# Kernel optimization log

Hardware: AMD Instinct MI355X
Metric: run time of the kernel (lower is better)

The kernel has to match this reference:

```python
import jax, jax.numpy as jnp
import numpy as np

N = 50000
E = 400000
IN_CH = 256
HEADS = 4
OUT_CH = 64
HID = HEADS * OUT_CH  # 256
ALPHA = 0.2
LN_EPS = 1e-5


def setup_inputs() -> dict:
    key = jax.random.key(0)
    ks = jax.random.split(key, 8)
    h = jax.random.normal(ks[0], (N, IN_CH), dtype=jnp.float32)
    edge_row = jax.random.randint(ks[1], (E,), 0, N, dtype=jnp.int32)
    edge_col = jax.random.randint(ks[2], (E,), 0, N, dtype=jnp.int32)
    # xavier-uniform-ish params
    def xavier(k, shape, fan_in, fan_out):
        lim = np.sqrt(6.0 / (fan_in + fan_out)).astype(np.float32)
        return jax.random.uniform(k, shape, jnp.float32, -lim, lim)
    W = xavier(ks[3], (IN_CH, HID), IN_CH, HID)              # Linear no bias
    attn_fc = xavier(ks[4], (HEADS, 2 * OUT_CH), 2 * OUT_CH, 1)
    ln_gamma = jnp.ones((HID,), jnp.float32)
    ln_beta = jnp.zeros((HID,), jnp.float32)
    ffn_w = xavier(ks[5], (HID, HID), HID, HID)
    ffn_b = jnp.zeros((HID,), jnp.float32)
    return {"h": h, "edge_row": edge_row, "edge_col": edge_col,
            "W": W, "attn_fc": attn_fc, "ln_gamma": ln_gamma,
            "ln_beta": ln_beta, "ffn_w": ffn_w, "ffn_b": ffn_b}


def reference(h, edge_row, edge_col, W, attn_fc, ln_gamma, ln_beta, ffn_w, ffn_b):
    # Wh: [N, H, D]
    Wh = (h @ W).reshape(N, HEADS, OUT_CH)
    Wh_i = Wh[edge_row]   # [E, H, D]
    Wh_j = Wh[edge_col]   # [E, H, D]
    # e = leakyrelu(cat(Wh_i, Wh_j) . attn_fc) per head -> split contraction
    a_src = attn_fc[:, :OUT_CH]  # [H, D]
    a_dst = attn_fc[:, OUT_CH:]  # [H, D]
    e = jnp.einsum('ehd,hd->eh', Wh_i, a_src) + jnp.einsum('ehd,hd->eh', Wh_j, a_dst)
    e = jax.nn.leaky_relu(e, negative_slope=ALPHA)
    # global max-shift exp (matches torch.exp(e - e.max(dim=0)))
    e = jnp.exp(e - jnp.max(e, axis=0, keepdims=True))  # [E, H]
    e_sum = jax.ops.segment_sum(e, edge_row, num_segments=N)  # [N, H]
    alpha = e / (e_sum[edge_row] + 1e-15)  # [E, H]  (dropout = identity in eval)
    # scatter-add weighted messages
    h_new = jax.ops.segment_sum(Wh_j * alpha[..., None], edge_row, num_segments=N)
    h_new = h_new.reshape(N, HID) + Wh.reshape(N, HID)  # residual (shapes match)
    # LayerNorm
    mu = jnp.mean(h_new, axis=-1, keepdims=True)
    var = jnp.var(h_new, axis=-1, keepdims=True)
    h_new = (h_new - mu) * jax.lax.rsqrt(var + LN_EPS) * ln_gamma + ln_beta
    # FFN: Linear + ReLU (+ dropout identity)
    return jax.nn.relu(h_new @ ffn_w + ffn_b)
```

## Files before the change

### kernel.cpp

```cpp
#include <hip/hip_runtime.h>
#include <hip/hip_bf16.h>

#define N_NODES 50000
#define E_EDGES 400000
#define IN_CH   256
#define HEADS   4
#define OUT_CH  64
#define HID     256
#define ALPHA   0.2f
#define LN_EPS  1e-5f

using f32x4  = __attribute__((ext_vector_type(4))) float;
using bf16x8 = __attribute__((ext_vector_type(8))) short;
using u16x8  = __attribute__((ext_vector_type(8))) unsigned short;
using u16x4  = __attribute__((ext_vector_type(4))) unsigned short;

__device__ __forceinline__ unsigned short f2bf(float f) {
    __hip_bfloat16 b = __float2bfloat16(f);
    return *(unsigned short*)&b;
}
__device__ __forceinline__ float bf2f(unsigned short u) {
    __hip_bfloat16 b = *(__hip_bfloat16*)&u;
    return __bfloat162float(b);
}

__global__ __launch_bounds__(256) void prep_kernel(
    const float* __restrict__ W, const float* __restrict__ ffn_w,
    unsigned short* __restrict__ Wt, unsigned short* __restrict__ Ft)
{
    int i = blockIdx.x * 256 + threadIdx.x;
    if (i < 65536) {
        int n = i >> 8, k = i & 255;
        Wt[i] = f2bf(W[k * 256 + n]);
    } else {
        int j = i - 65536;
        int n = j >> 8, k = j & 255;
        Ft[j] = f2bf(ffn_w[k * 256 + n]);
    }
}

template<bool A_IS_F32, bool RELU_BIAS>
__global__ __launch_bounds__(256) void gemm_mfma(
    const void* __restrict__ Av, const unsigned short* __restrict__ Bt,
    const float* __restrict__ bias, void* __restrict__ Cv, int M)
{
    constexpr int K = 256, BM = 128, BK = 64;
    __shared__ unsigned short As[BM * BK];
    __shared__ unsigned short Bs[BM * BK];

    const int bx = blockIdx.x & 1;
    const int by = blockIdx.x >> 1;
    const int row0 = by * BM, col0 = bx * 128;
    const int tid = threadIdx.x;
    const int lane = tid & 63, wid = tid >> 6;
    const int wr = wid >> 1, wc = wid & 1;
    const int lm = lane & 15, lk = lane >> 4;

    f32x4 acc[4][4] = {};

    for (int k0 = 0; k0 < K; k0 += BK) {
        if (A_IS_F32) {
            const float* A = (const float*)Av;
            #pragma unroll
            for (int i = 0; i < 8; i++) {
                int lin = tid + i * 256;
                int r = lin >> 4, c4 = lin & 15;
                int gr = row0 + r;
                float4 v = make_float4(0.f, 0.f, 0.f, 0.f);
                if (gr < M) v = *(const float4*)(A + (size_t)gr * K + k0 + c4 * 4);
                uint2 p;
                p.x = (unsigned)f2bf(v.x) | ((unsigned)f2bf(v.y) << 16);
                p.y = (unsigned)f2bf(v.z) | ((unsigned)f2bf(v.w) << 16);
                *(uint2*)((char*)As + r * 128 + ((c4 * 8) ^ ((r & 7) << 4))) = p;
            }
        } else {
            const unsigned short* A = (const unsigned short*)Av;
            #pragma unroll
            for (int i = 0; i < 4; i++) {
                int lin = tid + i * 256;
                int r = lin >> 3, c8 = lin & 7;
                int gr = row0 + r;
                u16x8 v = {};
                if (gr < M) v = *(const u16x8*)(A + (size_t)gr * K + k0 + c8 * 8);
                *(u16x8*)((char*)As + r * 128 + ((c8 * 16) ^ ((r & 7) << 4))) = v;
            }
        }
        #pragma unroll
        for (int i = 0; i < 4; i++) {
            int lin = tid + i * 256;
            int r = lin >> 3, c8 = lin & 7;
            u16x8 v = *(const u16x8*)(Bt + (size_t)(col0 + r) * K + k0 + c8 * 8);
            *(u16x8*)((char*)Bs + r * 128 + ((c8 * 16) ^ ((r & 7) << 4))) = v;
        }
        __syncthreads();

        #pragma unroll
        for (int kk = 0; kk < 2; kk++) {
            bf16x8 a[4], b[4];
            #pragma unroll
            for (int i = 0; i < 4; i++) {
                int m = wr * 64 + i * 16 + lm;
                a[i] = *(const bf16x8*)((const char*)As + m * 128 +
                        ((kk * 64 + lk * 16) ^ ((m & 7) << 4)));
            }
            #pragma unroll
            for (int j = 0; j < 4; j++) {
                int n = wc * 64 + j * 16 + lm;
                b[j] = *(const bf16x8*)((const char*)Bs + n * 128 +
                        ((kk * 64 + lk * 16) ^ ((n & 7) << 4)));
            }
            #pragma unroll
            for (int i = 0; i < 4; i++)
                #pragma unroll
                for (int j = 0; j < 4; j++)
                    acc[i][j] = __builtin_amdgcn_mfma_f32_16x16x32_bf16(
                        a[i], b[j], acc[i][j], 0, 0, 0);
        }
        __syncthreads();
    }

    #pragma unroll
    for (int j = 0; j < 4; j++) {
        int gc = col0 + wc * 64 + j * 16 + lm;
        float bv = RELU_BIAS ? bias[gc] : 0.f;
        #pragma unroll
        for (int i = 0; i < 4; i++) {
            int gr0 = row0 + wr * 64 + i * 16 + lk * 4;
            #pragma unroll
            for (int q = 0; q < 4; q++) {
                int gr = gr0 + q;
                if (gr >= M) continue;
                float v = acc[i][j][q];
                if (RELU_BIAS) {
                    v += bv; v = v > 0.f ? v : 0.f;
                    ((float*)Cv)[(size_t)gr * 256 + gc] = v;
                } else {
                    ((unsigned short*)Cv)[(size_t)gr * 256 + gc] = f2bf(v);
                }
            }
        }
    }
}

__global__ __launch_bounds__(256) void scores_kernel(
    const unsigned short* __restrict__ Wh, const float* __restrict__ attn_fc,
    float* __restrict__ s_src, float* __restrict__ s_dst)
{
    const int lane = threadIdx.x & 63, wid = threadIdx.x >> 6;
    const int n = blockIdx.x * 4 + wid;
    const int h = lane >> 4;
    const int d0 = 4 * (lane & 15);
    u16x4 w = *(const u16x4*)(Wh + (size_t)n * HID + 4 * lane);
    float ps = 0.f, pd = 0.f;
    #pragma unroll
    for (int q = 0; q < 4; q++) {
        float wf = bf2f(w[q]);
        ps += wf * attn_fc[h * 128 + d0 + q];
        pd += wf * attn_fc[h * 128 + 64 + d0 + q];
    }
    #pragma unroll
    for (int off = 8; off; off >>= 1) {
        ps += __shfl_xor(ps, off, 16);
        pd += __shfl_xor(pd, off, 16);
    }
    if ((lane & 15) == 0) {
        s_src[n * HEADS + h] = ps;
        s_dst[n * HEADS + h] = pd;
    }
}

__global__ void hist_kernel(const int* __restrict__ erow, int* __restrict__ counts) {
    int e = blockIdx.x * blockDim.x + threadIdx.x;
    if (e < E_EDGES) atomicAdd(&counts[erow[e]], 1);
}

__global__ __launch_bounds__(256) void scanA_kernel(
    const int* __restrict__ counts, int* __restrict__ bsum)
{
    const int b = blockIdx.x, tid = threadIdx.x;
    int i0 = b * 512 + tid;
    int v = 0;
    if (i0 < N_NODES) v += counts[i0];
    if (i0 + 256 < N_NODES) v += counts[i0 + 256];
    #pragma unroll
    for (int off = 32; off; off >>= 1) v += __shfl_xor(v, off, 64);
    __shared__ int ws[4];
    if ((tid & 63) == 0) ws[tid >> 6] = v;
    __syncthreads();
    if (tid == 0) bsum[b] = ws[0] + ws[1] + ws[2] + ws[3];
}

__global__ __launch_bounds__(128) void scanB_kernel(
    const int* __restrict__ bsum, int* __restrict__ bscan, int nb)
{
    const int tid = threadIdx.x;
    const int lane = tid & 63, wid = tid >> 6;
    int val = (tid < nb) ? bsum[tid] : 0;
    int x = val;
    #pragma unroll
    for (int off = 1; off < 64; off <<= 1) {
        int y = __shfl_up(x, off, 64);
        if (lane >= off) x += y;
    }
    __shared__ int w0;
    if (tid == 63) w0 = x;
    __syncthreads();
    if (wid == 1) x += w0;
    if (tid < nb) bscan[tid] = x - val;
}

__global__ __launch_bounds__(512) void scanC_kernel(
    const int* __restrict__ counts, const int* __restrict__ bscan,
    int* __restrict__ offsets, int* __restrict__ cursor)
{
    const int b = blockIdx.x, tid = threadIdx.x;
    const int lane = tid & 63, wid = tid >> 6;
    const int i = b * 512 + tid;
    int v = (i < N_NODES) ? counts[i] : 0;
    int x = v;
    #pragma unroll
    for (int off = 1; off < 64; off <<= 1) {
        int y = __shfl_up(x, off, 64);
        if (lane >= off) x += y;
    }
    __shared__ int ws[8];
    if (lane == 63) ws[wid] = x;
    __syncthreads();
    if (wid == 0 && lane < 8) {
        int s = ws[lane];
        #pragma unroll
        for (int off = 1; off < 8; off <<= 1) {
            int y = __shfl_up(s, off, 8);
            if ((lane & 7) >= off) s += y;
        }
        ws[lane] = s;
    }
    __syncthreads();
    int prefix = (wid ? ws[wid - 1] : 0) + bscan[b];
    int excl = prefix + x - v;
    if (i < N_NODES) { offsets[i] = excl; cursor[i] = excl; }
    if (i == N_NODES - 1) offsets[N_NODES] = excl + v;
}

__global__ __launch_bounds__(256) void scatter_kernel(
    const int* __restrict__ erow, const int* __restrict__ ecol,
    const float* __restrict__ s_src, const float* __restrict__ s_dst,
    int* __restrict__ cursor, int* __restrict__ sorted_col,
    float4* __restrict__ sorted_w)
{
    int e = blockIdx.x * blockDim.x + threadIdx.x;
    if (e >= E_EDGES) return;
    int r = erow[e], c = ecol[e];
    float4 ss = ((const float4*)s_src)[r];
    float4 sd = ((const float4*)s_dst)[c];
    float sc[4] = {ss.x + sd.x, ss.y + sd.y, ss.z + sd.z, ss.w + sd.w};
    float4 w;
    float* wp = (float*)&w;
    #pragma unroll
    for (int h = 0; h < 4; h++) {
        float v = sc[h] > 0.f ? sc[h] : ALPHA * sc[h];
        wp[h] = __expf(v);
    }
    int pos = atomicAdd(&cursor[r], 1);
    sorted_col[pos] = c;
    sorted_w[pos] = w;
}

__global__ __launch_bounds__(256) void aggregate_ln_kernel(
    const unsigned short* __restrict__ Wh, const float* __restrict__ sorted_w,
    const int* __restrict__ offsets, const int* __restrict__ sorted_col,
    const float* __restrict__ ln_gamma, const float* __restrict__ ln_beta,
    unsigned short* __restrict__ h_ln)
{
    const int lane = threadIdx.x & 63, wid = threadIdx.x >> 6;
    const int n = blockIdx.x * 4 + wid;
    const int h = lane >> 4;
    const int c0 = 4 * lane;
    const int beg = offsets[n], end = offsets[n + 1];

    float acc[4] = {0.f, 0.f, 0.f, 0.f};
    float wsum = 0.f;
    for (int base = beg; base < end; base += 64) {
        int cnt = min(64, end - base);
        int cv = (base + lane < end) ? sorted_col[base + lane] : 0;
        #pragma unroll 2
        for (int jj = 0; jj < cnt; jj++) {
            float w = sorted_w[(base + jj) * 4 + h];
            int c = __shfl(cv, jj, 64);
            u16x4 wr = *(const u16x4*)(Wh + (size_t)c * HID + c0);
            wsum += w;
            #pragma unroll
            for (int q = 0; q < 4; q++) acc[q] += w * bf2f(wr[q]);
        }
    }
    u16x4 rr = *(const u16x4*)(Wh + (size_t)n * HID + c0);
    float inv_w = 1.f / (wsum + 1e-15f);
    float val[4];
    #pragma unroll
    for (int q = 0; q < 4; q++) val[q] = acc[q] * inv_w + bf2f(rr[q]);

    float s = val[0] + val[1] + val[2] + val[3];
    #pragma unroll
    for (int off = 32; off; off >>= 1) s += __shfl_xor(s, off, 64);
    float mu = s * (1.f / HID);
    float s2 = 0.f;
    #pragma unroll
    for (int q = 0; q < 4; q++) { float d = val[q] - mu; s2 += d * d; }
    #pragma unroll
    for (int off = 32; off; off >>= 1) s2 += __shfl_xor(s2, off, 64);
    float inv_std = rsqrtf(s2 * (1.f / HID) + LN_EPS);

    float4 g = *(const float4*)(ln_gamma + c0);
    float4 bb = *(const float4*)(ln_beta + c0);
    u16x4 outv;
    outv[0] = f2bf((val[0] - mu) * inv_std * g.x + bb.x);
    outv[1] = f2bf((val[1] - mu) * inv_std * g.y + bb.y);
    outv[2] = f2bf((val[2] - mu) * inv_std * g.z + bb.z);
    outv[3] = f2bf((val[3] - mu) * inv_std * g.w + bb.w);
    *(u16x4*)(h_ln + (size_t)n * HID + c0) = outv;
}

extern "C" void kernel_launch(void* const* d_in, const int* in_sizes, int n_in,
                              void* d_out, int out_size, void* d_ws, size_t ws_size,
                              hipStream_t stream)
{
    const float* h        = (const float*)d_in[0];
    const int*   erow     = (const int*)  d_in[1];
    const int*   ecol     = (const int*)  d_in[2];
    const float* W        = (const float*)d_in[3];
    const float* attn_fc  = (const float*)d_in[4];
    const float* ln_gamma = (const float*)d_in[5];
    const float* ln_beta  = (const float*)d_in[6];
    const float* ffn_w    = (const float*)d_in[7];
    const float* ffn_b    = (const float*)d_in[8];
    float* out = (float*)d_out;

    unsigned short* Wh   = (unsigned short*)d_ws;
    unsigned short* h_ln = Wh + (size_t)N_NODES * HID;
    unsigned short* Wt   = h_ln + (size_t)N_NODES * HID;
    unsigned short* Ft   = Wt + 65536;
    float* s_src  = (float*)(Ft + 65536);
    float* s_dst  = s_src + N_NODES * HEADS;
    float* sorted_w = s_dst + N_NODES * HEADS;
    int*   counts = (int*)(sorted_w + (size_t)E_EDGES * HEADS);
    int*   offsets = counts + N_NODES;
    int*   cursor  = offsets + N_NODES + 1;
    int*   sorted_col = cursor + N_NODES;
    int*   bsum   = sorted_col + E_EDGES;
    int*   bscan  = bsum + 128;

    const int NB = (N_NODES + 511) / 512;

    hipMemsetAsync(counts, 0, N_NODES * sizeof(int), stream);
    prep_kernel<<<512, 256, 0, stream>>>(W, ffn_w, Wt, Ft);

    gemm_mfma<true, false><<<((N_NODES + 127) / 128) * 2, 256, 0, stream>>>(
        h, Wt, nullptr, Wh, N_NODES);

    scores_kernel<<<N_NODES / 4, 256, 0, stream>>>(Wh, attn_fc, s_src, s_dst);
    hist_kernel<<<(E_EDGES + 255) / 256, 256, 0, stream>>>(erow, counts);
    scanA_kernel<<<NB, 256, 0, stream>>>(counts, bsum);
    scanB_kernel<<<1, 128, 0, stream>>>(bsum, bscan, NB);
    scanC_kernel<<<NB, 512, 0, stream>>>(counts, bscan, offsets, cursor);
    scatter_kernel<<<(E_EDGES + 255) / 256, 256, 0, stream>>>(
        erow, ecol, s_src, s_dst, cursor, sorted_col, (float4*)sorted_w);
    aggregate_ln_kernel<<<N_NODES / 4, 256, 0, stream>>>(
        Wh, sorted_w, offsets, sorted_col, ln_gamma, ln_beta, h_ln);

    gemm_mfma<false, true><<<((N_NODES + 127) / 128) * 2, 256, 0, stream>>>(
        h_ln, Ft, ffn_b, out, N_NODES);
}
```

Before: 281.6 us.

## Fuse attention score computation into GEMM epilogue and double-buffer LDS with direct loads

```diff
diff --git a/kernel.cpp b/kernel.cpp
--- a/kernel.cpp
+++ b/kernel.cpp
@@ -15,6 +15,9 @@
 using u16x8  = __attribute__((ext_vector_type(8))) unsigned short;
 using u16x4  = __attribute__((ext_vector_type(4))) unsigned short;
 
+typedef __attribute__((address_space(3))) void* lds_vp;
+typedef const __attribute__((address_space(1))) void* gbl_vp;
+
 __device__ __forceinline__ unsigned short f2bf(float f) {
     __hip_bfloat16 b = __float2bfloat16(f);
     return *(unsigned short*)&b;
@@ -39,18 +42,20 @@
     }
 }
 
-template<bool A_IS_F32, bool RELU_BIAS>
+template<bool A_IS_F32, bool RELU_BIAS, bool SCORES>
 __global__ __launch_bounds__(256) void gemm_mfma(
     const void* __restrict__ Av, const unsigned short* __restrict__ Bt,
-    const float* __restrict__ bias, void* __restrict__ Cv, int M)
-{
-    constexpr int K = 256, BM = 128, BK = 64;
-    __shared__ unsigned short As[BM * BK];
-    __shared__ unsigned short Bs[BM * BK];
+    const float* __restrict__ bias, const float* __restrict__ attn_fc,
+    void* __restrict__ Cv, float* __restrict__ s_src, float* __restrict__ s_dst,
+    int M)
+{
+    constexpr int K = 256, BK = 64, NT = K / BK;
+    __shared__ unsigned short As[2][128 * 64];
+    __shared__ unsigned short Bs[2][128 * 64];
 
     const int bx = blockIdx.x & 1;
     const int by = blockIdx.x >> 1;
-    const int row0 = by * BM, col0 = bx * 128;
+    const int row0 = by * 128, col0 = bx * 128;
     const int tid = threadIdx.x;
     const int lane = tid & 63, wid = tid >> 6;
     const int wr = wid >> 1, wc = wid & 1;
@@ -58,55 +63,62 @@
 
     f32x4 acc[4][4] = {};
 
-    for (int k0 = 0; k0 < K; k0 += BK) {
-        if (A_IS_F32) {
-            const float* A = (const float*)Av;
-            #pragma unroll
-            for (int i = 0; i < 8; i++) {
-                int lin = tid + i * 256;
-                int r = lin >> 4, c4 = lin & 15;
-                int gr = row0 + r;
-                float4 v = make_float4(0.f, 0.f, 0.f, 0.f);
-                if (gr < M) v = *(const float4*)(A + (size_t)gr * K + k0 + c4 * 4);
-                uint2 p;
-                p.x = (unsigned)f2bf(v.x) | ((unsigned)f2bf(v.y) << 16);
-                p.y = (unsigned)f2bf(v.z) | ((unsigned)f2bf(v.w) << 16);
-                *(uint2*)((char*)As + r * 128 + ((c4 * 8) ^ ((r & 7) << 4))) = p;
-            }
-        } else {
-            const unsigned short* A = (const unsigned short*)Av;
-            #pragma unroll
-            for (int i = 0; i < 4; i++) {
-                int lin = tid + i * 256;
-                int r = lin >> 3, c8 = lin & 7;
-                int gr = row0 + r;
-                u16x8 v = {};
-                if (gr < M) v = *(const u16x8*)(A + (size_t)gr * K + k0 + c8 * 8);
-                *(u16x8*)((char*)As + r * 128 + ((c8 * 16) ^ ((r & 7) << 4))) = v;
-            }
-        }
+    auto stageB = [&](int buf, int k0) {
         #pragma unroll
         for (int i = 0; i < 4; i++) {
+            int lin = wid * 64 + lane + i * 256;
+            int r = lin >> 3, c8 = lin & 7;
+            int c8s = c8 ^ (r & 7);
+            const unsigned short* g = Bt + (size_t)(col0 + r) * K + k0 + c8s * 8;
+            __builtin_amdgcn_global_load_lds((gbl_vp)g,
+                (lds_vp)&Bs[buf][(size_t)(i * 256 + wid * 64) * 8], 16, 0, 0);
+        }
+    };
+    auto stageA_bf16 = [&](int buf, int k0) {
+        const unsigned short* A = (const unsigned short*)Av;
+        #pragma unroll
+        for (int i = 0; i < 4; i++) {
+            int lin = wid * 64 + lane + i * 256;
+            int r = lin >> 3, c8 = lin & 7;
+            int c8s = c8 ^ (r & 7);
+            const unsigned short* g = A + (size_t)(row0 + r) * K + k0 + c8s * 8;
+            __builtin_amdgcn_global_load_lds((gbl_vp)g,
+                (lds_vp)&As[buf][(size_t)(i * 256 + wid * 64) * 8], 16, 0, 0);
+        }
+    };
+    auto stageA_f32 = [&](int buf, int k0) {
+        const float* A = (const float*)Av;
+        #pragma unroll
+        for (int i = 0; i < 8; i++) {
             int lin = tid + i * 256;
-            int r = lin >> 3, c8 = lin & 7;
-            u16x8 v = *(const u16x8*)(Bt + (size_t)(col0 + r) * K + k0 + c8 * 8);
-            *(u16x8*)((char*)Bs + r * 128 + ((c8 * 16) ^ ((r & 7) << 4))) = v;
-        }
-        __syncthreads();
-
+            int r = lin >> 4, c4 = lin & 15;
+            int gr = row0 + r;
+            float4 v = make_float4(0.f, 0.f, 0.f, 0.f);
+            if (gr < M) v = *(const float4*)(A + (size_t)gr * K + k0 + c4 * 4);
+            uint2 p;
+            p.x = (unsigned)f2bf(v.x) | ((unsigned)f2bf(v.y) << 16);
+            p.y = (unsigned)f2bf(v.z) | ((unsigned)f2bf(v.w) << 16);
+            *(uint2*)((char*)&As[buf][0] + r * 128 + ((c4 * 8) ^ ((r & 7) << 4))) = p;
+        }
+    };
+    auto stage = [&](int buf, int k0) {
+        if (A_IS_F32) stageA_f32(buf, k0); else stageA_bf16(buf, k0);
+        stageB(buf, k0);
+    };
+    auto compute = [&](int buf) {
         #pragma unroll
         for (int kk = 0; kk < 2; kk++) {
             bf16x8 a[4], b[4];
             #pragma unroll
             for (int i = 0; i < 4; i++) {
                 int m = wr * 64 + i * 16 + lm;
-                a[i] = *(const bf16x8*)((const char*)As + m * 128 +
+                a[i] = *(const bf16x8*)((const char*)&As[buf][0] + m * 128 +
                         ((kk * 64 + lk * 16) ^ ((m & 7) << 4)));
             }
             #pragma unroll
             for (int j = 0; j < 4; j++) {
                 int n = wc * 64 + j * 16 + lm;
-                b[j] = *(const bf16x8*)((const char*)Bs + n * 128 +
+                b[j] = *(const bf16x8*)((const char*)&Bs[buf][0] + n * 128 +
                         ((kk * 64 + lk * 16) ^ ((n & 7) << 4)));
             }
             #pragma unroll
@@ -116,6 +128,14 @@
                     acc[i][j] = __builtin_amdgcn_mfma_f32_16x16x32_bf16(
                         a[i], b[j], acc[i][j], 0, 0, 0);
         }
+    };
+
+    stage(0, 0);
+    __syncthreads();
+    #pragma unroll
+    for (int t = 0; t < NT; t++) {
+        if (t + 1 < NT) stage((t + 1) & 1, (t + 1) * BK);
+        compute(t & 1);
         __syncthreads();
     }
 
@@ -140,32 +160,37 @@
             }
         }
     }
-}
-
-__global__ __launch_bounds__(256) void scores_kernel(
-    const unsigned short* __restrict__ Wh, const float* __restrict__ attn_fc,
-    float* __restrict__ s_src, float* __restrict__ s_dst)
-{
-    const int lane = threadIdx.x & 63, wid = threadIdx.x >> 6;
-    const int n = blockIdx.x * 4 + wid;
-    const int h = lane >> 4;
-    const int d0 = 4 * (lane & 15);
-    u16x4 w = *(const u16x4*)(Wh + (size_t)n * HID + 4 * lane);
-    float ps = 0.f, pd = 0.f;
-    #pragma unroll
-    for (int q = 0; q < 4; q++) {
-        float wf = bf2f(w[q]);
-        ps += wf * attn_fc[h * 128 + d0 + q];
-        pd += wf * attn_fc[h * 128 + 64 + d0 + q];
-    }
-    #pragma unroll
-    for (int off = 8; off; off >>= 1) {
-        ps += __shfl_xor(ps, off, 16);
-        pd += __shfl_xor(pd, off, 16);
-    }
-    if ((lane & 15) == 0) {
-        s_src[n * HEADS + h] = ps;
-        s_dst[n * HEADS + h] = pd;
+
+    if (SCORES) {
+        const int head = bx * 2 + wc;
+        float as[4], ad[4];
+        #pragma unroll
+        for (int j = 0; j < 4; j++) {
+            as[j] = attn_fc[head * 128 + j * 16 + lm];
+            ad[j] = attn_fc[head * 128 + 64 + j * 16 + lm];
+        }
+        #pragma unroll
+        for (int i = 0; i < 4; i++) {
+            #pragma unroll
+            for (int q = 0; q < 4; q++) {
+                float ps = 0.f, pd = 0.f;
+                #pragma unroll
+                for (int j = 0; j < 4; j++) {
+                    ps += acc[i][j][q] * as[j];
+                    pd += acc[i][j][q] * ad[j];
+                }
+                #pragma unroll
+                for (int off = 8; off; off >>= 1) {
+                    ps += __shfl_xor(ps, off, 16);
+                    pd += __shfl_xor(pd, off, 16);
+                }
+                int gr = row0 + wr * 64 + i * 16 + lk * 4 + q;
+                if (lm == 0 && gr < M) {
+                    s_src[gr * HEADS + head] = ps;
+                    s_dst[gr * HEADS + head] = pd;
+                }
+            }
+        }
     }
 }
 
@@ -354,10 +379,9 @@
     hipMemsetAsync(counts, 0, N_NODES * sizeof(int), stream);
     prep_kernel<<<512, 256, 0, stream>>>(W, ffn_w, Wt, Ft);
 
-    gemm_mfma<true, false><<<((N_NODES + 127) / 128) * 2, 256, 0, stream>>>(
-        h, Wt, nullptr, Wh, N_NODES);
-
-    scores_kernel<<<N_NODES / 4, 256, 0, stream>>>(Wh, attn_fc, s_src, s_dst);
+    gemm_mfma<true, false, true><<<((N_NODES + 127) / 128) * 2, 256, 0, stream>>>(
+        h, Wt, nullptr, attn_fc, Wh, s_src, s_dst, N_NODES);
+
     hist_kernel<<<(E_EDGES + 255) / 256, 256, 0, stream>>>(erow, counts);
     scanA_kernel<<<NB, 256, 0, stream>>>(counts, bsum);
     scanB_kernel<<<1, 128, 0, stream>>>(bsum, bscan, NB);
@@ -367,6 +391,6 @@
     aggregate_ln_kernel<<<N_NODES / 4, 256, 0, stream>>>(
         Wh, sorted_w, offsets, sorted_col, ln_gamma, ln_beta, h_ln);
 
-    gemm_mfma<false, true><<<((N_NODES + 127) / 128) * 2, 256, 0, stream>>>(
-        h_ln, Ft, ffn_b, out, N_NODES);
-}
+    gemm_mfma<false, true, false><<<((N_NODES + 127) / 128) * 2, 256, 0, stream>>>(
+        h_ln, Ft, ffn_b, nullptr, out, nullptr, nullptr, N_NODES);
+}
```

New measurement: 276.5 us. No clear change (-1.8%).

## Use persistent B-resident MFMA GEMM and process two edges per wave in aggregation

Applied to the files above, without the earlier changes.

```diff
diff --git a/kernel.cpp b/kernel.cpp
--- a/kernel.cpp
+++ b/kernel.cpp
@@ -10,10 +10,13 @@
 #define ALPHA   0.2f
 #define LN_EPS  1e-5f
 
-using f32x4  = __attribute__((ext_vector_type(4))) float;
+using f32x16 = __attribute__((ext_vector_type(16))) float;
 using bf16x8 = __attribute__((ext_vector_type(8))) short;
 using u16x8  = __attribute__((ext_vector_type(8))) unsigned short;
 using u16x4  = __attribute__((ext_vector_type(4))) unsigned short;
+
+typedef __attribute__((address_space(3))) void* lds_vp;
+typedef const __attribute__((address_space(1))) void* gbl_vp;
 
 __device__ __forceinline__ unsigned short f2bf(float f) {
     __hip_bfloat16 b = __float2bfloat16(f);
@@ -40,103 +43,92 @@
 }
 
 template<bool A_IS_F32, bool RELU_BIAS>
-__global__ __launch_bounds__(256) void gemm_mfma(
+__global__ __launch_bounds__(512, 2) void gemm_bres(
     const void* __restrict__ Av, const unsigned short* __restrict__ Bt,
     const float* __restrict__ bias, void* __restrict__ Cv, int M)
 {
-    constexpr int K = 256, BM = 128, BK = 64;
-    __shared__ unsigned short As[BM * BK];
-    __shared__ unsigned short Bs[BM * BK];
-
-    const int bx = blockIdx.x & 1;
-    const int by = blockIdx.x >> 1;
-    const int row0 = by * BM, col0 = bx * 128;
+    __shared__ unsigned short Bs[256 * 256];
+
     const int tid = threadIdx.x;
     const int lane = tid & 63, wid = tid >> 6;
-    const int wr = wid >> 1, wc = wid & 1;
-    const int lm = lane & 15, lk = lane >> 4;
-
-    f32x4 acc[4][4] = {};
-
-    for (int k0 = 0; k0 < K; k0 += BK) {
+
+    #pragma unroll
+    for (int i = 0; i < 16; i++) {
+        int d = i * 512 + tid;
+        int n = d >> 5, cp = d & 31;
+        int cs = cp ^ (n & 31);
+        const unsigned short* g = Bt + (size_t)n * 256 + cs * 8;
+        __builtin_amdgcn_global_load_lds((gbl_vp)g, (lds_vp)&Bs[(size_t)d * 8],
+                                         16, 0, 0);
+    }
+    __syncthreads();
+
+    const int strip = wid * 256 + blockIdx.x;
+    const int r0 = strip * 32;
+    if (r0 >= M) return;
+
+    const int q5 = lane & 31, kg = lane >> 5;
+    const int rowc = min(r0 + q5, M - 1);
+
+    f32x16 acc[8] = {};
+
+    const float* Af = (const float*)Av;
+    const unsigned short* Ab = (const unsigned short*)Av;
+
+    float4 ra0, ra1; u16x8 rab;
+    if (A_IS_F32) {
+        const float* p = Af + (size_t)rowc * 256 + kg * 8;
+        ra0 = *(const float4*)p; ra1 = *(const float4*)(p + 4);
+    } else {
+        rab = *(const u16x8*)(Ab + (size_t)rowc * 256 + kg * 8);
+    }
+
+    #pragma unroll 2
+    for (int t = 0; t < 16; t++) {
+        float4 nb0, nb1; u16x8 nbb;
+        if (t + 1 < 16) {
+            if (A_IS_F32) {
+                const float* p = Af + (size_t)rowc * 256 + (t + 1) * 16 + kg * 8;
+                nb0 = *(const float4*)p; nb1 = *(const float4*)(p + 4);
+            } else {
+                nbb = *(const u16x8*)(Ab + (size_t)rowc * 256 + (t + 1) * 16 + kg * 8);
+            }
+        }
+        bf16x8 af;
         if (A_IS_F32) {
-            const float* A = (const float*)Av;
-            #pragma unroll
-            for (int i = 0; i < 8; i++) {
-                int lin = tid + i * 256;
-                int r = lin >> 4, c4 = lin & 15;
-                int gr = row0 + r;
-                float4 v = make_float4(0.f, 0.f, 0.f, 0.f);
-                if (gr < M) v = *(const float4*)(A + (size_t)gr * K + k0 + c4 * 4);
-                uint2 p;
-                p.x = (unsigned)f2bf(v.x) | ((unsigned)f2bf(v.y) << 16);
-                p.y = (unsigned)f2bf(v.z) | ((unsigned)f2bf(v.w) << 16);
-                *(uint2*)((char*)As + r * 128 + ((c4 * 8) ^ ((r & 7) << 4))) = p;
-            }
+            union { unsigned int u[4]; bf16x8 v; } cv;
+            cv.u[0] = (unsigned)f2bf(ra0.x) | ((unsigned)f2bf(ra0.y) << 16);
+            cv.u[1] = (unsigned)f2bf(ra0.z) | ((unsigned)f2bf(ra0.w) << 16);
+            cv.u[2] = (unsigned)f2bf(ra1.x) | ((unsigned)f2bf(ra1.y) << 16);
+            cv.u[3] = (unsigned)f2bf(ra1.z) | ((unsigned)f2bf(ra1.w) << 16);
+            af = cv.v;
         } else {
-            const unsigned short* A = (const unsigned short*)Av;
-            #pragma unroll
-            for (int i = 0; i < 4; i++) {
-                int lin = tid + i * 256;
-                int r = lin >> 3, c8 = lin & 7;
-                int gr = row0 + r;
-                u16x8 v = {};
-                if (gr < M) v = *(const u16x8*)(A + (size_t)gr * K + k0 + c8 * 8);
-                *(u16x8*)((char*)As + r * 128 + ((c8 * 16) ^ ((r & 7) << 4))) = v;
-            }
+            union { u16x8 u; bf16x8 v; } cv; cv.u = rab; af = cv.v;
         }
         #pragma unroll
-        for (int i = 0; i < 4; i++) {
-            int lin = tid + i * 256;
-            int r = lin >> 3, c8 = lin & 7;
-            u16x8 v = *(const u16x8*)(Bt + (size_t)(col0 + r) * K + k0 + c8 * 8);
-            *(u16x8*)((char*)Bs + r * 128 + ((c8 * 16) ^ ((r & 7) << 4))) = v;
-        }
-        __syncthreads();
-
-        #pragma unroll
-        for (int kk = 0; kk < 2; kk++) {
-            bf16x8 a[4], b[4];
-            #pragma unroll
-            for (int i = 0; i < 4; i++) {
-                int m = wr * 64 + i * 16 + lm;
-                a[i] = *(const bf16x8*)((const char*)As + m * 128 +
-                        ((kk * 64 + lk * 16) ^ ((m & 7) << 4)));
-            }
-            #pragma unroll
-            for (int j = 0; j < 4; j++) {
-                int n = wc * 64 + j * 16 + lm;
-                b[j] = *(const bf16x8*)((const char*)Bs + n * 128 +
-                        ((kk * 64 + lk * 16) ^ ((n & 7) << 4)));
-            }
-            #pragma unroll
-            for (int i = 0; i < 4; i++)
-                #pragma unroll
-                for (int j = 0; j < 4; j++)
-                    acc[i][j] = __builtin_amdgcn_mfma_f32_16x16x32_bf16(
-                        a[i], b[j], acc[i][j], 0, 0, 0);
-        }
-        __syncthreads();
-    }
-
-    #pragma unroll
-    for (int j = 0; j < 4; j++) {
-        int gc = col0 + wc * 64 + j * 16 + lm;
+        for (int n = 0; n < 8; n++) {
+            const bf16x8 bf = *(const bf16x8*)((const char*)Bs +
+                (size_t)(n * 32 + q5) * 512 + (((t * 2 + kg) ^ q5) * 16));
+            acc[n] = __builtin_amdgcn_mfma_f32_32x32x16_bf16(af, bf, acc[n], 0, 0, 0);
+        }
+        ra0 = nb0; ra1 = nb1; rab = nbb;
+    }
+
+    #pragma unroll
+    for (int n = 0; n < 8; n++) {
+        int gc = n * 32 + q5;
         float bv = RELU_BIAS ? bias[gc] : 0.f;
         #pragma unroll
-        for (int i = 0; i < 4; i++) {
-            int gr0 = row0 + wr * 64 + i * 16 + lk * 4;
-            #pragma unroll
-            for (int q = 0; q < 4; q++) {
-                int gr = gr0 + q;
-                if (gr >= M) continue;
-                float v = acc[i][j][q];
-                if (RELU_BIAS) {
-                    v += bv; v = v > 0.f ? v : 0.f;
-                    ((float*)Cv)[(size_t)gr * 256 + gc] = v;
-                } else {
-                    ((unsigned short*)Cv)[(size_t)gr * 256 + gc] = f2bf(v);
-                }
+        for (int reg = 0; reg < 16; reg++) {
+            int rl = (reg & 3) + 8 * (reg >> 2) + 4 * kg;
+            int gr = r0 + rl;
+            if (gr >= M) continue;
+            float v = acc[n][reg];
+            if (RELU_BIAS) {
+                v += bv; v = v > 0.f ? v : 0.f;
+                ((float*)Cv)[(size_t)gr * 256 + gc] = v;
+            } else {
+                ((unsigned short*)Cv)[(size_t)gr * 256 + gc] = f2bf(v);
             }
         }
     }
@@ -274,50 +266,77 @@
 {
     const int lane = threadIdx.x & 63, wid = threadIdx.x >> 6;
     const int n = blockIdx.x * 4 + wid;
-    const int h = lane >> 4;
-    const int c0 = 4 * lane;
+    const int p = lane >> 5;
+    const int q5 = lane & 31;
+    const int c0 = q5 * 8;
+    const int h = q5 >> 3;
     const int beg = offsets[n], end = offsets[n + 1];
 
-    float acc[4] = {0.f, 0.f, 0.f, 0.f};
+    float acc[8] = {};
     float wsum = 0.f;
     for (int base = beg; base < end; base += 64) {
         int cnt = min(64, end - base);
         int cv = (base + lane < end) ? sorted_col[base + lane] : 0;
+        int jj = 0;
         #pragma unroll 2
-        for (int jj = 0; jj < cnt; jj++) {
-            float w = sorted_w[(base + jj) * 4 + h];
-            int c = __shfl(cv, jj, 64);
-            u16x4 wr = *(const u16x4*)(Wh + (size_t)c * HID + c0);
+        for (; jj + 2 <= cnt; jj += 2) {
+            int c = __shfl(cv, jj + p, 64);
+            float w = sorted_w[(size_t)(base + jj + p) * 4 + h];
+            u16x8 r = *(const u16x8*)(Wh + (size_t)c * HID + c0);
             wsum += w;
             #pragma unroll
-            for (int q = 0; q < 4; q++) acc[q] += w * bf2f(wr[q]);
-        }
-    }
-    u16x4 rr = *(const u16x4*)(Wh + (size_t)n * HID + c0);
+            for (int k = 0; k < 8; k++) acc[k] += w * bf2f(r[k]);
+        }
+        if (jj < cnt) {
+            int c = __shfl(cv, jj, 64);
+            if (p == 0) {
+                float w = sorted_w[(size_t)(base + jj) * 4 + h];
+                u16x8 r = *(const u16x8*)(Wh + (size_t)c * HID + c0);
+                wsum += w;
+                #pragma unroll
+                for (int k = 0; k < 8; k++) acc[k] += w * bf2f(r[k]);
+            }
+        }
+    }
+    wsum += __shfl_xor(wsum, 32, 64);
+    #pragma unroll
+    for (int k = 0; k < 8; k++) acc[k] += __shfl_xor(acc[k], 32, 64);
+
+    u16x8 rr = *(const u16x8*)(Wh + (size_t)n * HID + c0);
     float inv_w = 1.f / (wsum + 1e-15f);
-    float val[4];
-    #pragma unroll
-    for (int q = 0; q < 4; q++) val[q] = acc[q] * inv_w + bf2f(rr[q]);
-
-    float s = val[0] + val[1] + val[2] + val[3];
-    #pragma unroll
-    for (int off = 32; off; off >>= 1) s += __shfl_xor(s, off, 64);
+    float val[8];
+    float s = 0.f;
+    #pragma unroll
+    for (int k = 0; k < 8; k++) {
+        val[k] = acc[k] * inv_w + bf2f(rr[k]);
+        s += val[k];
+    }
+    #pragma unroll
+    for (int off = 16; off; off >>= 1) s += __shfl_xor(s, off, 64);
     float mu = s * (1.f / HID);
     float s2 = 0.f;
     #pragma unroll
-    for (int q = 0; q < 4; q++) { float d = val[q] - mu; s2 += d * d; }
-    #pragma unroll
-    for (int off = 32; off; off >>= 1) s2 += __shfl_xor(s2, off, 64);
+    for (int k = 0; k < 8; k++) { float d = val[k] - mu; s2 += d * d; }
+    #pragma unroll
+    for (int off = 16; off; off >>= 1) s2 += __shfl_xor(s2, off, 64);
     float inv_std = rsqrtf(s2 * (1.f / HID) + LN_EPS);
 
-    float4 g = *(const float4*)(ln_gamma + c0);
-    float4 bb = *(const float4*)(ln_beta + c0);
-    u16x4 outv;
-    outv[0] = f2bf((val[0] - mu) * inv_std * g.x + bb.x);
-    outv[1] = f2bf((val[1] - mu) * inv_std * g.y + bb.y);
-    outv[2] = f2bf((val[2] - mu) * inv_std * g.z + bb.z);
-    outv[3] = f2bf((val[3] - mu) * inv_std * g.w + bb.w);
-    *(u16x4*)(h_ln + (size_t)n * HID + c0) = outv;
+    if (p == 0) {
+        float4 g0 = *(const float4*)(ln_gamma + c0);
+        float4 g1 = *(const float4*)(ln_gamma + c0 + 4);
+        float4 b0 = *(const float4*)(ln_beta + c0);
+        float4 b1 = *(const float4*)(ln_beta + c0 + 4);
+        u16x8 outv;
+        outv[0] = f2bf((val[0] - mu) * inv_std * g0.x + b0.x);
+        outv[1] = f2bf((val[1] - mu) * inv_std * g0.y + b0.y);
+        outv[2] = f2bf((val[2] - mu) * inv_std * g0.z + b0.z);
+        outv[3] = f2bf((val[3] - mu) * inv_std * g0.w + b0.w);
+        outv[4] = f2bf((val[4] - mu) * inv_std * g1.x + b1.x);
+        outv[5] = f2bf((val[5] - mu) * inv_std * g1.y + b1.y);
+        outv[6] = f2bf((val[6] - mu) * inv_std * g1.z + b1.z);
+        outv[7] = f2bf((val[7] - mu) * inv_std * g1.w + b1.w);
+        *(u16x8*)(h_ln + (size_t)n * HID + c0) = outv;
+    }
 }
 
 extern "C" void kernel_launch(void* const* d_in, const int* in_sizes, int n_in,
@@ -354,8 +373,7 @@
     hipMemsetAsync(counts, 0, N_NODES * sizeof(int), stream);
     prep_kernel<<<512, 256, 0, stream>>>(W, ffn_w, Wt, Ft);
 
-    gemm_mfma<true, false><<<((N_NODES + 127) / 128) * 2, 256, 0, stream>>>(
-        h, Wt, nullptr, Wh, N_NODES);
+    gemm_bres<true, false><<<256, 512, 0, stream>>>(h, Wt, nullptr, Wh, N_NODES);
 
     scores_kernel<<<N_NODES / 4, 256, 0, stream>>>(Wh, attn_fc, s_src, s_dst);
     hist_kernel<<<(E_EDGES + 255) / 256, 256, 0, stream>>>(erow, counts);
@@ -367,6 +385,5 @@
     aggregate_ln_kernel<<<N_NODES / 4, 256, 0, stream>>>(
         Wh, sorted_w, offsets, sorted_col, ln_gamma, ln_beta, h_ln);
 
-    gemm_mfma<false, true><<<((N_NODES + 127) / 128) * 2, 256, 0, stream>>>(
-        h_ln, Ft, ffn_b, out, N_NODES);
-}
+    gemm_bres<false, true><<<256, 512, 0, stream>>>(h_ln, Ft, ffn_b, out, N_NODES);
+}
```

Result: faster. 249.3 us (-11.4%).
